# Optimization experiments

Hardware: AMD Instinct MI355X
Metric: run time of the kernel (lower is better)

Reference implementation:

```python
import jax, jax.numpy as jnp
import numpy as np
from jax import lax

BIG = 1e10  # initial distance, matching torch's 1e10


def farthest_point_sample(xyz, init_farthest, npoint):
    """xyz: [B,N,3] float; init_farthest: [B] int32; returns centroids [B,npoint] int32."""
    B, N, _ = xyz.shape
    batch_idx = jnp.arange(B)

    def body(i, state):
        centroids, distance, farthest = state
        centroids = centroids.at[:, i].set(farthest)
        c = xyz[batch_idx, farthest][:, None, :]              # [B,1,3] current centroid
        dist = jnp.sum(jnp.square(xyz - c), axis=-1)          # [B,N] sq. distance
        distance = jnp.minimum(distance, dist)                # mask-update: keep min dist to any centroid
        farthest = jnp.argmax(distance, axis=-1).astype(jnp.int32)
        return centroids, distance, farthest

    centroids0 = jnp.zeros((B, npoint), jnp.int32)
    distance0 = jnp.full((B, N), BIG, xyz.dtype)
    centroids, _, _ = lax.fori_loop(0, npoint, body, (centroids0, distance0, init_farthest.astype(jnp.int32)))
    return centroids


def setup_inputs() -> dict:
    key = jax.random.key(0)
    k1, k2, k3 = jax.random.split(key, 3)
    B, N = 16, 100000
    mesh = jax.random.normal(k1, (B, N, 3), dtype=jnp.float32)
    contact_map = jax.random.uniform(k2, (B, N, 1), dtype=jnp.float32)
    init_farthest = jax.random.randint(k3, (B,), 0, N, dtype=jnp.int32)
    return {"mesh": mesh, "contact_map": contact_map, "init_farthest": init_farthest, "npoint": 1024}


def reference(mesh, contact_map, init_farthest, npoint):
    B, N, _ = mesh.shape
    batch_idx = jnp.arange(B)

    # __compute_mesh_scale: max distance from centroid, per batch
    centroid = jnp.mean(mesh, axis=1, keepdims=True)                      # [B,1,3]
    s_obj = jnp.max(jnp.sqrt(jnp.sum(jnp.square(mesh - centroid), axis=2)), axis=1)  # [B]

    # __farthest_point_sample
    centroids = farthest_point_sample(mesh, init_farthest, npoint)        # [B,npoint]

    # gather sampled points and contact values
    point_cloud = mesh[batch_idx[:, None], centroids]                     # [B,npoint,3]
    cm_sampled = contact_map[batch_idx[:, None], centroids]               # [B,npoint,1]

    # normalize by object scale (broadcast over points/coords)
    point_cloud_norm = point_cloud / s_obj[:, None, None]

    # point_cloud_norm_contact fed to the contact encoder in the original
    return jnp.concatenate([cm_sampled, point_cloud_norm], axis=2)        # [B,npoint,4]
```

## Files before the change

### kernel.cpp

```cpp
#include <hip/hip_runtime.h>
#include <cstdint>

#define NBATCH 16
#define NPOINT 1024
#define NPTS   100000
#define GPB    16
#define TPB    256
#define WPB    4
#define NSUB   16
#define STRIDE (GPB * TPB)
#define KPT    25
#define NPAIR  13

typedef unsigned long long u64;


__global__ __launch_bounds__(256) void sum_kernel(const float* __restrict__ xyz,
                                                  float* __restrict__ psum) {
    const int b   = blockIdx.x & 15;
    const int sub = blockIdx.x >> 4;
    const float* P = xyz + (size_t)b * NPTS * 3;
    float sx = 0.f, sy = 0.f, sz = 0.f;
    for (int i = sub * TPB + threadIdx.x; i < NPTS; i += NSUB * TPB) {
        sx += P[i * 3 + 0];
        sy += P[i * 3 + 1];
        sz += P[i * 3 + 2];
    }
    #pragma unroll
    for (int off = 32; off; off >>= 1) {
        sx += __shfl_xor(sx, off);
        sy += __shfl_xor(sy, off);
        sz += __shfl_xor(sz, off);
    }
    __shared__ float r[3][4];
    const int wave = threadIdx.x >> 6, lane = threadIdx.x & 63;
    if (lane == 0) { r[0][wave] = sx; r[1][wave] = sy; r[2][wave] = sz; }
    __syncthreads();
    if (threadIdx.x == 0) {
        float* o = psum + (b * NSUB + sub) * 4;
        o[0] = r[0][0] + r[0][1] + r[0][2] + r[0][3];
        o[1] = r[1][0] + r[1][1] + r[1][2] + r[1][3];
        o[2] = r[2][0] + r[2][1] + r[2][2] + r[2][3];
    }
}

__global__ __launch_bounds__(256) void max_kernel(const float* __restrict__ xyz,
                                                  const float* __restrict__ psum,
                                                  unsigned* __restrict__ pmax,
                                                  u64* __restrict__ slots) {
    if (blockIdx.x == 0) {
        slots[threadIdx.x] = 0ull;
        slots[threadIdx.x + 256] = 0ull;
    }
    const int b   = blockIdx.x & 15;
    const int sub = blockIdx.x >> 4;
    const float* P = xyz + (size_t)b * NPTS * 3;
    float sx = 0.f, sy = 0.f, sz = 0.f;
    #pragma unroll
    for (int s = 0; s < NSUB; ++s) {
        sx += psum[(b * NSUB + s) * 4 + 0];
        sy += psum[(b * NSUB + s) * 4 + 1];
        sz += psum[(b * NSUB + s) * 4 + 2];
    }
    const float mx = sx / (float)NPTS, my = sy / (float)NPTS, mz = sz / (float)NPTS;
    float best = 0.f;
    for (int i = sub * TPB + threadIdx.x; i < NPTS; i += NSUB * TPB) {
        float dx = P[i * 3 + 0] - mx;
        float dy = P[i * 3 + 1] - my;
        float dz = P[i * 3 + 2] - mz;
        best = fmaxf(best, dx * dx + dy * dy + dz * dz);
    }
    #pragma unroll
    for (int off = 32; off; off >>= 1) best = fmaxf(best, __shfl_xor(best, off));
    __shared__ float r[4];
    const int wave = threadIdx.x >> 6, lane = threadIdx.x & 63;
    if (lane == 0) r[wave] = best;
    __syncthreads();
    if (threadIdx.x == 0)
        pmax[b * NSUB + sub] = __float_as_uint(fmaxf(fmaxf(r[0], r[1]), fmaxf(r[2], r[3])));
}

__global__ __launch_bounds__(256, 1) void fps_kernel(const float* __restrict__ xyz,
                                                     const float* __restrict__ cmap,
                                                     const int* __restrict__ init_far,
                                                     const unsigned* __restrict__ pmax,
                                                     u64* __restrict__ slots,
                                                     float* __restrict__ out) {
    const int b   = blockIdx.x & 15;
    const int g   = blockIdx.x >> 4;
    const int tid = threadIdx.x;
    const int wave = tid >> 6, lane = tid & 63;
    const int tl  = g * TPB + tid;
    const float* P = xyz + (size_t)b * NPTS * 3;

    float m0 = 0.f;
    #pragma unroll
    for (int s = 0; s < NSUB; ++s) m0 = fmaxf(m0, __uint_as_float(pmax[b * NSUB + s]));
    const float sb = sqrtf(m0);

    float pxx[NPAIR], pxy[NPAIR], pyx[NPAIR], pyy[NPAIR],
          pzx[NPAIR], pzy[NPAIR], pdx[NPAIR], pdy[NPAIR];
    #pragma unroll
    for (int j = 0; j < NPAIR; ++j) {
        const int p0 = tl + (2 * j) * STRIDE;
        const int p1 = tl + (2 * j + 1) * STRIDE;
        const bool v0 = p0 < NPTS, v1 = p1 < NPTS;
        pxx[j] = v0 ? P[p0 * 3 + 0] : 0.f;  pxy[j] = v1 ? P[p1 * 3 + 0] : 0.f;
        pyx[j] = v0 ? P[p0 * 3 + 1] : 0.f;  pyy[j] = v1 ? P[p1 * 3 + 1] : 0.f;
        pzx[j] = v0 ? P[p0 * 3 + 2] : 0.f;  pzy[j] = v1 ? P[p1 * 3 + 2] : 0.f;
        pdx[j] = v0 ? 1e10f : -1.0f;        pdy[j] = v1 ? 1e10f : -1.0f;
    }

    __shared__ u64 lds_key[WPB];
    __shared__ int lds_win;
    __shared__ int curhist[NPOINT];

    int cur = init_far[b];
    float cx = P[cur * 3 + 0], cy = P[cur * 3 + 1], cz = P[cur * 3 + 2];

    for (int i = 0; i < NPOINT; ++i) {
        if (tid == 192) curhist[i] = cur;
        if (i == NPOINT - 1) break;

        float best = -1.0f;
        int bidx = 0;
        {
            #pragma clang fp contract(off)
            #pragma unroll
            for (int j = 0; j < NPAIR; ++j) {
                float dx0 = pxx[j] - cx, dx1 = pxy[j] - cx;
                float dy0 = pyx[j] - cy, dy1 = pyy[j] - cy;
                float dz0 = pzx[j] - cz, dz1 = pzy[j] - cz;
                float s0 = dx0 * dx0 + dy0 * dy0;  float s1 = dx1 * dx1 + dy1 * dy1;
                s0 = s0 + dz0 * dz0;               s1 = s1 + dz1 * dz1;
                float n0 = fminf(pdx[j], s0);      float n1 = fminf(pdy[j], s1);
                pdx[j] = n0;                       pdy[j] = n1;
                if (n0 > best) { best = n0; bidx = tl + (2 * j) * STRIDE; }
                if (n1 > best) { best = n1; bidx = tl + (2 * j + 1) * STRIDE; }
            }
        }

        const u64 want = (u64)(i + 1);
        u64 key = ((u64)__float_as_uint(best) << 22) | (u64)(0x3FFFFFu - (unsigned)bidx);
        #pragma unroll
        for (int off = 32; off; off >>= 1) {
            u64 o2 = __shfl_xor(key, off);
            key = o2 > key ? o2 : key;
        }
        if (lane == 0) lds_key[wave] = key;
        __syncthreads();

        u64* const bs = slots + ((size_t)(i & 1) * NBATCH + b) * GPB;

        if (wave == 0) {
            u64 bk = (lane < WPB) ? lds_key[lane] : 0;
            #pragma unroll
            for (int off = 1; off < WPB; off <<= 1) {
                u64 o2 = __shfl_xor(bk, off);
                bk = o2 > bk ? o2 : bk;
            }
            if (lane == 0)
                __hip_atomic_store(&bs[g], bk | (want << 54),
                                   __ATOMIC_RELAXED, __HIP_MEMORY_SCOPE_AGENT);

            u64 v = 0;
            if (lane < GPB) {
                u64* sp = &bs[lane];
                int tries = 0;
                for (;;) {
                    v = __hip_atomic_load(sp, __ATOMIC_RELAXED, __HIP_MEMORY_SCOPE_AGENT);
                    if ((v >> 54) >= want) break;
                    if (++tries > 16) __builtin_amdgcn_s_sleep(1);
                }
            }
            #pragma unroll
            for (int off = 8; off; off >>= 1) {
                u64 o2 = __shfl_xor(v, off);
                v = o2 > v ? o2 : v;
            }
            if (lane == 0)
                lds_win = (int)(0x3FFFFFu - (unsigned)(v & 0x3FFFFFu));
        }
        __syncthreads();
        cur = lds_win;
        cx = P[cur * 3 + 0];
        cy = P[cur * 3 + 1];
        cz = P[cur * 3 + 2];
    }

    __syncthreads();
    if (tid < 64) {
        const int row = g * 64 + tid;
        const int c   = curhist[row];
        const float cm = cmap[(size_t)b * NPTS + c];
        const float x = P[c * 3 + 0], y = P[c * 3 + 1], z = P[c * 3 + 2];
        float* o = out + ((size_t)b * NPOINT + row) * 4;
        o[0] = cm;
        o[1] = x / sb;
        o[2] = y / sb;
        o[3] = z / sb;
    }
}

extern "C" void kernel_launch(void* const* d_in, const int* in_sizes, int n_in,
                              void* d_out, int out_size, void* d_ws, size_t ws_size,
                              hipStream_t stream) {
    const float* mesh = (const float*)d_in[0];
    const float* cmap = (const float*)d_in[1];
    const int* init   = (const int*)d_in[2];
    float* out = (float*)d_out;

    char* ws      = (char*)d_ws;
    float* psum   = (float*)ws;
    unsigned* pmx = (unsigned*)(ws + 4096);
    u64* slots    = (u64*)(ws + 8192);

    sum_kernel<<<dim3(256), dim3(TPB), 0, stream>>>(mesh, psum);
    max_kernel<<<dim3(256), dim3(TPB), 0, stream>>>(mesh, psum, pmx, slots);
    fps_kernel<<<dim3(256), dim3(TPB), 0, stream>>>(mesh, cmap, init, pmx, slots, out);
}
```

Measured before the change: 1.991 ms.

## Replace block barriers with per-wave global slot exchange and DPP reductions

Each wave now publishes its own argmax key to a global slot array sized for 64 agents per batch, and every wave independently polls all 64 slots and reduces them. This removes both __syncthreads and the LDS hop per FPS iteration. Wave-level max reductions use DPP row shifts/broadcasts plus a readlane from lane 63 instead of shfl_xor. The trade-off is four times more polling traffic on global memory per iteration and more slots to zero.

```diff
diff --git a/kernel.cpp b/kernel.cpp
--- a/kernel.cpp
+++ b/kernel.cpp
@@ -7,12 +7,14 @@
 #define GPB    16
 #define TPB    256
 #define WPB    4
+#define NAG    64
 #define NSUB   16
 #define STRIDE (GPB * TPB)
 #define KPT    25
 #define NPAIR  13
 
 typedef unsigned long long u64;
+typedef unsigned int u32;
 
 
 __global__ __launch_bounds__(256) void sum_kernel(const float* __restrict__ xyz,
@@ -49,8 +51,8 @@
                                                   unsigned* __restrict__ pmax,
                                                   u64* __restrict__ slots) {
     if (blockIdx.x == 0) {
-        slots[threadIdx.x] = 0ull;
-        slots[threadIdx.x + 256] = 0ull;
+        #pragma unroll
+        for (int k = 0; k < 8; ++k) slots[threadIdx.x + 256 * k] = 0ull;
     }
     const int b   = blockIdx.x & 15;
     const int sub = blockIdx.x >> 4;
@@ -78,6 +80,31 @@
     __syncthreads();
     if (threadIdx.x == 0)
         pmax[b * NSUB + sub] = __float_as_uint(fmaxf(fmaxf(r[0], r[1]), fmaxf(r[2], r[3])));
+}
+
+__device__ __forceinline__ u64 wave_max_u64(u64 k) {
+    u32 lo = (u32)k, hi = (u32)(k >> 32);
+    #define DPP_STEP(CTRL) do {                                                          \
+        u32 olo = (u32)__builtin_amdgcn_update_dpp((int)lo, (int)lo, CTRL, 0xf, 0xf, false); \
+        u32 ohi = (u32)__builtin_amdgcn_update_dpp((int)hi, (int)hi, CTRL, 0xf, 0xf, false); \
+        u64 oo = ((u64)ohi << 32) | olo;                                                 \
+        u64 cc = ((u64)hi  << 32) | lo;                                                  \
+        if (oo > cc) { lo = olo; hi = ohi; }                                             \
+    } while (0)
+    DPP_STEP(0x111);
+    DPP_STEP(0x112);
+    DPP_STEP(0x114);
+    DPP_STEP(0x118);
+    DPP_STEP(0x142);
+    DPP_STEP(0x143);
+    #undef DPP_STEP
+    return ((u64)hi << 32) | lo;
+}
+
+__device__ __forceinline__ u64 bcast_lane63(u64 v) {
+    u32 lo = (u32)__builtin_amdgcn_readlane((int)(u32)v, 63);
+    u32 hi = (u32)__builtin_amdgcn_readlane((int)(u32)(v >> 32), 63);
+    return ((u64)hi << 32) | lo;
 }
 
 __global__ __launch_bounds__(256, 1) void fps_kernel(const float* __restrict__ xyz,
@@ -90,6 +117,7 @@
     const int g   = blockIdx.x >> 4;
     const int tid = threadIdx.x;
     const int wave = tid >> 6, lane = tid & 63;
+    const int ag  = g * WPB + wave;
     const int tl  = g * TPB + tid;
     const float* P = xyz + (size_t)b * NPTS * 3;
 
@@ -111,8 +139,6 @@
         pdx[j] = v0 ? 1e10f : -1.0f;        pdy[j] = v1 ? 1e10f : -1.0f;
     }
 
-    __shared__ u64 lds_key[WPB];
-    __shared__ int lds_win;
     __shared__ int curhist[NPOINT];
 
     int cur = init_far[b];
@@ -142,47 +168,26 @@
 
         const u64 want = (u64)(i + 1);
         u64 key = ((u64)__float_as_uint(best) << 22) | (u64)(0x3FFFFFu - (unsigned)bidx);
-        #pragma unroll
-        for (int off = 32; off; off >>= 1) {
-            u64 o2 = __shfl_xor(key, off);
-            key = o2 > key ? o2 : key;
+        u64 r = wave_max_u64(key);
+
+        u64* const bs = slots + ((size_t)(i & 1) * NBATCH + b) * NAG;
+        if (lane == 63)
+            __hip_atomic_store(&bs[ag], r | (want << 54),
+                               __ATOMIC_RELAXED, __HIP_MEMORY_SCOPE_AGENT);
+
+        u64 v;
+        {
+            u64* sp = &bs[lane];
+            int tries = 0;
+            for (;;) {
+                v = __hip_atomic_load(sp, __ATOMIC_RELAXED, __HIP_MEMORY_SCOPE_AGENT);
+                if (__all((v >> 54) >= want)) break;
+                if (++tries > 16) __builtin_amdgcn_s_sleep(1);
+            }
         }
-        if (lane == 0) lds_key[wave] = key;
-        __syncthreads();
-
-        u64* const bs = slots + ((size_t)(i & 1) * NBATCH + b) * GPB;
-
-        if (wave == 0) {
-            u64 bk = (lane < WPB) ? lds_key[lane] : 0;
-            #pragma unroll
-            for (int off = 1; off < WPB; off <<= 1) {
-                u64 o2 = __shfl_xor(bk, off);
-                bk = o2 > bk ? o2 : bk;
-            }
-            if (lane == 0)
-                __hip_atomic_store(&bs[g], bk | (want << 54),
-                                   __ATOMIC_RELAXED, __HIP_MEMORY_SCOPE_AGENT);
-
-            u64 v = 0;
-            if (lane < GPB) {
-                u64* sp = &bs[lane];
-                int tries = 0;
-                for (;;) {
-                    v = __hip_atomic_load(sp, __ATOMIC_RELAXED, __HIP_MEMORY_SCOPE_AGENT);
-                    if ((v >> 54) >= want) break;
-                    if (++tries > 16) __builtin_amdgcn_s_sleep(1);
-                }
-            }
-            #pragma unroll
-            for (int off = 8; off; off >>= 1) {
-                u64 o2 = __shfl_xor(v, off);
-                v = o2 > v ? o2 : v;
-            }
-            if (lane == 0)
-                lds_win = (int)(0x3FFFFFu - (unsigned)(v & 0x3FFFFFu));
-        }
-        __syncthreads();
-        cur = lds_win;
+
+        u64 w = bcast_lane63(wave_max_u64(v));
+        cur = (int)(0x3FFFFFu - (unsigned)(w & 0x3FFFFFu));
         cx = P[cur * 3 + 0];
         cy = P[cur * 3 + 1];
         cz = P[cur * 3 + 2];
```

Result: slower. 4.987 ms (+150.4%).
